# Optimization experiments

Measured on AMD Instinct MI355X. Metric: run time of the kernel, lower is better.

The kernel has to match this reference:

```python
import jax, jax.numpy as jnp
import numpy as np

N = 50000   # nodes
E = 640000  # edges
G = 256     # graphs
IN = 32     # in_channels
H = 128     # hidden_channels
L = 5       # num GENConv layers
LH = 64     # lstm hidden
OUT = 10    # out_channels
EPS_GEN = 1e-7

def _bn(x, g, b, eps=1e-5):
    # BatchNorm1d in training mode: biased batch stats over node dim
    mu = x.mean(0)
    var = x.var(0)
    return (x - mu) * jax.lax.rsqrt(var + eps) * g + b

def _genconv(x, eattr, src, dst, w1, b1, g1, bb1, w2, b2):
    # message: relu(x_j + edge_attr) + eps   [E, H]
    msg = jax.nn.relu(x[src] + eattr) + EPS_GEN
    # softmax aggregation (t=1) per destination node, per channel
    m = jax.ops.segment_max(msg, dst, num_segments=N)
    e = jnp.exp(msg - m[dst])
    s = jax.ops.segment_sum(e, dst, num_segments=N)
    alpha = e / s[dst]
    agg = jax.ops.segment_sum(alpha * msg, dst, num_segments=N)
    out = agg + x
    # MLP: Linear(H,2H) -> BN -> ReLU -> Linear(2H,H)
    hmid = jax.nn.relu(_bn(out @ w1.T + b1, g1, bb1))
    return hmid @ w2.T + b2

def setup_inputs() -> dict:
    key = jax.random.key(0)
    ks = jax.random.split(key, 16)
    s = 0.05
    inp = {}
    inp["x"] = jax.random.normal(ks[0], (N, IN), jnp.float32)
    inp["node_cycle_counts"] = jax.random.uniform(ks[1], (N, 8), jnp.float32)
    inp["edge_index"] = jax.random.randint(ks[2], (2, E), 0, N)
    inp["edge_attr"] = jax.random.randint(ks[3], (E,), 0, 4)
    inp["batch"] = jnp.sort(jax.random.randint(ks[4], (N,), 0, G))
    inp["fc_w"] = jax.random.normal(ks[5], (H, IN + 8), jnp.float32) * s
    inp["fc_b"] = jnp.zeros((H,), jnp.float32)
    inp["edge_emb"] = jax.random.normal(ks[6], (4, H), jnp.float32) * s
    inp["conv_w1"] = jax.random.normal(ks[7], (L, 2 * H, H), jnp.float32) * s
    inp["conv_b1"] = jnp.zeros((L, 2 * H), jnp.float32)
    inp["conv_bn_g"] = jnp.ones((L, 2 * H), jnp.float32)
    inp["conv_bn_b"] = jnp.zeros((L, 2 * H), jnp.float32)
    inp["conv_w2"] = jax.random.normal(ks[8], (L, H, 2 * H), jnp.float32) * s
    inp["conv_b2"] = jnp.zeros((L, H), jnp.float32)
    inp["bn_g"] = jnp.ones((L, H), jnp.float32)
    inp["bn_b"] = jnp.zeros((L, H), jnp.float32)
    inp["lstm_wih"] = jax.random.normal(ks[9], (4 * LH, H), jnp.float32) * s
    inp["lstm_whh"] = jax.random.normal(ks[10], (4 * LH, LH), jnp.float32) * s
    inp["lstm_bih"] = jnp.zeros((4 * LH,), jnp.float32)
    inp["lstm_bhh"] = jnp.zeros((4 * LH,), jnp.float32)
    inp["lin_w"] = jax.random.normal(ks[11], (OUT, LH), jnp.float32) * s
    inp["lin_b"] = jnp.zeros((OUT,), jnp.float32)
    return inp

def reference(x, node_cycle_counts, edge_index, edge_attr, batch,
              fc_w, fc_b, edge_emb, conv_w1, conv_b1, conv_bn_g, conv_bn_b,
              conv_w2, conv_b2, bn_g, bn_b,
              lstm_wih, lstm_whh, lstm_bih, lstm_bhh, lin_w, lin_b):
    src, dst = edge_index[0], edge_index[1]
    eattr = edge_emb[edge_attr]                              # [E, H]
    h = jnp.concatenate([x, node_cycle_counts], 1) @ fc_w.T + fc_b  # [N, H]
    for i in range(L):
        h = _genconv(h, eattr, src, dst, conv_w1[i], conv_b1[i],
                     conv_bn_g[i], conv_bn_b[i], conv_w2[i], conv_b2[i])
        h = jax.nn.relu(_bn(h, bn_g[i], bn_b[i]))
    p = jax.ops.segment_sum(h, batch, num_segments=G)        # global_add_pool [G, H]
    # single-step LSTM with h0 = c0 = 0
    gates = p @ lstm_wih.T + lstm_bih + lstm_bhh
    i_g, f_g, g_g, o_g = jnp.split(gates, 4, axis=1)
    c = jax.nn.sigmoid(i_g) * jnp.tanh(g_g)
    hh = jax.nn.sigmoid(o_g) * jnp.tanh(c)
    return hh @ lin_w.T + lin_b                              # [G, OUT]
```

## Files before the change

kernel.cpp:

```cpp
#include <hip/hip_runtime.h>
#include <hip/hip_bf16.h>
#include <math.h>

#define NNODES 50000
#define NEDGES 640000
#define NGRAPH 256
#define CIN 32
#define HD 128
#define NLAYER 5
#define LHID 64
#define COUT 10
#define EPS_GEN 1e-7f
#define INVN (1.f / (float)NNODES)
#define SCAN_BLOCKS 196

typedef __attribute__((ext_vector_type(8))) short short8;
typedef __attribute__((ext_vector_type(4))) float floatx4;

__device__ __forceinline__ unsigned short f2bf(float f) {
    union { float f; unsigned u; } v; v.f = f;
    unsigned r = v.u + 0x7FFFu + ((v.u >> 16) & 1u);
    return (unsigned short)(r >> 16);
}
__device__ __forceinline__ float bf2f(unsigned short h) {
    union { unsigned u; float f; } v; v.u = ((unsigned)h) << 16;
    return v.f;
}

__global__ void hist_kernel(const int* __restrict__ dst, int* __restrict__ deg, int e) {
    int i = blockIdx.x * blockDim.x + threadIdx.x;
    if (i < e) atomicAdd(&deg[dst[i]], 1);
}

__global__ void blocksum_kernel(const int* __restrict__ deg, int* __restrict__ bsum) {
    int i = blockIdx.x * 256 + threadIdx.x;
    int v = (i < NNODES) ? deg[i] : 0;
#pragma unroll
    for (int d = 32; d; d >>= 1) v += __shfl_down(v, d);
    __shared__ int ws4[4];
    if ((threadIdx.x & 63) == 0) ws4[threadIdx.x >> 6] = v;
    __syncthreads();
    if (threadIdx.x == 0) bsum[blockIdx.x] = ws4[0] + ws4[1] + ws4[2] + ws4[3];
}

__global__ void scanpartials_kernel(const int* __restrict__ bsum, int* __restrict__ bpre) {
    __shared__ int t[256];
    int i = threadIdx.x;
    t[i] = (i < SCAN_BLOCKS) ? bsum[i] : 0;
    __syncthreads();
    for (int d = 1; d < 256; d <<= 1) {
        int v = (i >= d) ? t[i - d] : 0;
        __syncthreads();
        t[i] += v;
        __syncthreads();
    }
    bpre[i] = (i == 0) ? 0 : t[i - 1];
}

__global__ void writeoff_kernel(const int* __restrict__ deg, const int* __restrict__ bpre,
                                int* __restrict__ off, int* __restrict__ cursor) {
    __shared__ int t[256];
    int tid = threadIdx.x;
    int i = blockIdx.x * 256 + tid;
    int v = (i < NNODES) ? deg[i] : 0;
    t[tid] = v;
    __syncthreads();
    for (int d = 1; d < 256; d <<= 1) {
        int u = (tid >= d) ? t[tid - d] : 0;
        __syncthreads();
        t[tid] += u;
        __syncthreads();
    }
    int excl = bpre[blockIdx.x] + t[tid] - v;
    if (i < NNODES) { off[i] = excl; cursor[i] = excl; }
    if (i == NNODES - 1) off[NNODES] = excl + v;
}

__global__ void scatter_kernel(const int* __restrict__ src, const int* __restrict__ dst,
                               const int* __restrict__ eattr, int* __restrict__ cursor,
                               int* __restrict__ pedge, int e) {
    int i = blockIdx.x * blockDim.x + threadIdx.x;
    if (i < e) {
        int slot = atomicAdd(&cursor[dst[i]], 1);
        pedge[slot] = src[i] | (eattr[i] << 27);
    }
}

__global__ void wsplit_kernel(const float* __restrict__ w1, const float* __restrict__ w2,
                              short* __restrict__ w1h, short* __restrict__ w1l,
                              short* __restrict__ w2h, short* __restrict__ w2l) {
    int i = blockIdx.x * 256 + threadIdx.x;
    if (i < NLAYER * 2 * HD * HD) {
        float v = w1[i];
        unsigned short hb = f2bf(v);
        w1h[i] = (short)hb;
        w1l[i] = (short)f2bf(v - bf2f(hb));
        float u = w2[i];
        unsigned short hb2 = f2bf(u);
        w2h[i] = (short)hb2;
        w2l[i] = (short)f2bf(u - bf2f(hb2));
    }
}

__global__ __launch_bounds__(256) void fc_kernel(
    const float* __restrict__ x, const float* __restrict__ ncc,
    const float* __restrict__ w, const float* __restrict__ b,
    float* __restrict__ h) {
    __shared__ float ws[HD][41];
    __shared__ float bs[HD];
    int tid = threadIdx.x;
    for (int i = tid; i < HD * 40; i += 256) ws[i / 40][i % 40] = w[i];
    if (tid < HD) bs[tid] = b[tid];
    __syncthreads();
    int c = tid & 127;
    int hi = tid >> 7;
#pragma unroll
    for (int nn = 0; nn < 4; ++nn) {
        int node = blockIdx.x * 8 + nn * 2 + hi;
        const float4* xr = reinterpret_cast<const float4*>(x + (size_t)node * CIN);
        const float4* nr = reinterpret_cast<const float4*>(ncc + (size_t)node * 8);
        float acc = bs[c];
#pragma unroll
        for (int k4 = 0; k4 < 8; ++k4) {
            float4 xv = xr[k4];
            acc += xv.x * ws[c][k4 * 4 + 0];
            acc += xv.y * ws[c][k4 * 4 + 1];
            acc += xv.z * ws[c][k4 * 4 + 2];
            acc += xv.w * ws[c][k4 * 4 + 3];
        }
#pragma unroll
        for (int k4 = 0; k4 < 2; ++k4) {
            float4 nv = nr[k4];
            acc += nv.x * ws[c][32 + k4 * 4 + 0];
            acc += nv.y * ws[c][32 + k4 * 4 + 1];
            acc += nv.z * ws[c][32 + k4 * 4 + 2];
            acc += nv.w * ws[c][32 + k4 * 4 + 3];
        }
        h[(size_t)node * HD + c] = acc;
    }
}

template <bool BN>
__global__ __launch_bounds__(256) void agg_kernel(
    const float* __restrict__ h, const int* __restrict__ off,
    const int* __restrict__ pedge, const float* __restrict__ edge_emb,
    const float* __restrict__ sums, const float* __restrict__ sqs,
    const float* __restrict__ g, const float* __restrict__ bb,
    short* __restrict__ x0h, short* __restrict__ x0l) {
    __shared__ float ee[4 * HD];
    __shared__ float scs[HD], shs[HD];
    int tid = threadIdx.x;
    ee[tid] = edge_emb[tid];
    ee[tid + 256] = edge_emb[tid + 256];
    if (BN && tid < HD) {
        float mu = sums[tid] * INVN;
        float var = fmaxf(sqs[tid] * INVN - mu * mu, 0.f);
        float is = rsqrtf(var + 1e-5f);
        float sc = g[tid] * is;
        scs[tid] = sc;
        shs[tid] = bb[tid] - mu * sc;
    }
    __syncthreads();

    int node = blockIdx.x * 4 + (tid >> 6);
    int lane = tid & 63;
    int half = lane >> 5;
    int c4 = (lane & 31) * 4;

    int b = off[node], e = off[node + 1];
    float4 sc4 = make_float4(1.f, 1.f, 1.f, 1.f);
    float4 sh4 = make_float4(0.f, 0.f, 0.f, 0.f);
    if (BN) {
        sc4 = *reinterpret_cast<const float4*>(&scs[c4]);
        sh4 = *reinterpret_cast<const float4*>(&shs[c4]);
    }
    float4 S = make_float4(0.f, 0.f, 0.f, 0.f);
    float4 T = make_float4(0.f, 0.f, 0.f, 0.f);
    int j = b + half;
    unsigned pnext = (j < e) ? (unsigned)pedge[j] : 0u;
    for (; j < e; j += 2) {
        unsigned p = pnext;
        if (j + 2 < e) pnext = (unsigned)pedge[j + 2];
        int s = p & 0x07FFFFFFu;
        int a = p >> 27;
        float4 v = *reinterpret_cast<const float4*>(&h[(size_t)s * HD + c4]);
        float4 ev = *reinterpret_cast<const float4*>(&ee[a * HD + c4]);
        if (BN) {
            v.x = fmaxf(fmaf(v.x, sc4.x, sh4.x), 0.f);
            v.y = fmaxf(fmaf(v.y, sc4.y, sh4.y), 0.f);
            v.z = fmaxf(fmaf(v.z, sc4.z, sh4.z), 0.f);
            v.w = fmaxf(fmaf(v.w, sc4.w, sh4.w), 0.f);
        }
        float m0 = fmaxf(v.x + ev.x, 0.f) + EPS_GEN;
        float m1 = fmaxf(v.y + ev.y, 0.f) + EPS_GEN;
        float m2 = fmaxf(v.z + ev.z, 0.f) + EPS_GEN;
        float m3 = fmaxf(v.w + ev.w, 0.f) + EPS_GEN;
        float e0 = __expf(m0), e1 = __expf(m1), e2 = __expf(m2), e3 = __expf(m3);
        S.x += e0; S.y += e1; S.z += e2; S.w += e3;
        T.x = fmaf(e0, m0, T.x); T.y = fmaf(e1, m1, T.y);
        T.z = fmaf(e2, m2, T.z); T.w = fmaf(e3, m3, T.w);
    }
    S.x += __shfl(S.x, lane ^ 32); S.y += __shfl(S.y, lane ^ 32);
    S.z += __shfl(S.z, lane ^ 32); S.w += __shfl(S.w, lane ^ 32);
    T.x += __shfl(T.x, lane ^ 32); T.y += __shfl(T.y, lane ^ 32);
    T.z += __shfl(T.z, lane ^ 32); T.w += __shfl(T.w, lane ^ 32);
    if (half == 0) {
        float4 r = *reinterpret_cast<const float4*>(&h[(size_t)node * HD + c4]);
        if (BN) {
            r.x = fmaxf(fmaf(r.x, sc4.x, sh4.x), 0.f);
            r.y = fmaxf(fmaf(r.y, sc4.y, sh4.y), 0.f);
            r.z = fmaxf(fmaf(r.z, sc4.z, sh4.z), 0.f);
            r.w = fmaxf(fmaf(r.w, sc4.w, sh4.w), 0.f);
        }
        if (e > b) {
            r.x += T.x / S.x; r.y += T.y / S.y;
            r.z += T.z / S.z; r.w += T.w / S.w;
        }
        float vv[4] = {r.x, r.y, r.z, r.w};
        short4 hv, lv;
        short hh4[4], ll4[4];
#pragma unroll
        for (int q = 0; q < 4; ++q) {
            unsigned short hb = f2bf(vv[q]);
            hh4[q] = (short)hb;
            ll4[q] = (short)f2bf(vv[q] - bf2f(hb));
        }
        hv.x = hh4[0]; hv.y = hh4[1]; hv.z = hh4[2]; hv.w = hh4[3];
        lv.x = ll4[0]; lv.y = ll4[1]; lv.z = ll4[2]; lv.w = ll4[3];
        *reinterpret_cast<short4*>(&x0h[(size_t)node * HD + c4]) = hv;
        *reinterpret_cast<short4*>(&x0l[(size_t)node * HD + c4]) = lv;
    }
}

template <int NPANEL, int KT, int NFULL, bool TRANS>
__global__ __launch_bounds__(256) void gemm_kernel(
    const short* __restrict__ Ahg, const short* __restrict__ Alg,
    const float* __restrict__ Afp,
    const short* __restrict__ Bhg, const short* __restrict__ Blg,
    const float* __restrict__ bias,
    const float* __restrict__ sums_in, const float* __restrict__ sqs_in,
    const float* __restrict__ g_in, const float* __restrict__ b_in,
    float* __restrict__ C, float* __restrict__ sums, float* __restrict__ sqs,
    int M) {
    constexpr int K = KT * 32;
    constexpr int BSTRIDE = K + 8;
    constexpr int NT = NPANEL / 16;
    __shared__ short Bs[2][NPANEL][BSTRIDE];
    __shared__ float scol[NPANEL], sqcol[NPANEL];
    __shared__ float sL[256], shL[256];
    int tid = threadIdx.x;
    int m0 = blockIdx.x * 128;
    int n0 = blockIdx.y * NPANEL;
    if (tid < NPANEL) { scol[tid] = 0.f; sqcol[tid] = 0.f; }
    if (TRANS && tid < K) {
        float mu = sums_in[tid] * INVN;
        float var = fmaxf(sqs_in[tid] * INVN - mu * mu, 0.f);
        float is = rsqrtf(var + 1e-5f);
        float sc = g_in[tid] * is;
        sL[tid] = sc;
        shL[tid] = b_in[tid] - mu * sc;
    }
    constexpr int ELEMS = NPANEL * (K / 8);
#pragma unroll
    for (int i = tid; i < ELEMS; i += 256) {
        int n = i / (K / 8);
        int k8 = (i % (K / 8)) * 8;
        *reinterpret_cast<short8*>(&Bs[0][n][k8]) =
            *reinterpret_cast<const short8*>(&Bhg[(size_t)(n0 + n) * K + k8]);
        *reinterpret_cast<short8*>(&Bs[1][n][k8]) =
            *reinterpret_cast<const short8*>(&Blg[(size_t)(n0 + n) * K + k8]);
    }
    __syncthreads();

    int wv = tid >> 6;
    int lane = tid & 63;
    int ml = lane & 15;
    int quad = lane >> 4;
    int mrow0 = m0 + wv * 32;

    floatx4 acc[2][NT];
#pragma unroll
    for (int mt = 0; mt < 2; ++mt)
#pragma unroll
        for (int nt = 0; nt < NT; ++nt) acc[mt][nt] = (floatx4){0.f, 0.f, 0.f, 0.f};

    int arow[2];
#pragma unroll
    for (int mt = 0; mt < 2; ++mt) arow[mt] = min(mrow0 + mt * 16 + ml, M - 1);

    if (!TRANS) {
        short8 ah[2][KT], al[2][KT];
#pragma unroll
        for (int mt = 0; mt < 2; ++mt)
#pragma unroll
            for (int kt = 0; kt < KT; ++kt) {
                size_t aoff = (size_t)arow[mt] * K + kt * 32 + quad * 8;
                ah[mt][kt] = *reinterpret_cast<const short8*>(&Ahg[aoff]);
                al[mt][kt] = *reinterpret_cast<const short8*>(&Alg[aoff]);
            }
#pragma unroll
        for (int kt = 0; kt < KT; ++kt)
#pragma unroll
            for (int nt = 0; nt < NT; ++nt) {
                short8 bh = *reinterpret_cast<const short8*>(&Bs[0][nt * 16 + ml][kt * 32 + quad * 8]);
                short8 bl = *reinterpret_cast<const short8*>(&Bs[1][nt * 16 + ml][kt * 32 + quad * 8]);
#pragma unroll
                for (int mt = 0; mt < 2; ++mt) {
                    acc[mt][nt] = __builtin_amdgcn_mfma_f32_16x16x32_bf16(ah[mt][kt], bh, acc[mt][nt], 0, 0, 0);
                    acc[mt][nt] = __builtin_amdgcn_mfma_f32_16x16x32_bf16(al[mt][kt], bh, acc[mt][nt], 0, 0, 0);
                    acc[mt][nt] = __builtin_amdgcn_mfma_f32_16x16x32_bf16(ah[mt][kt], bl, acc[mt][nt], 0, 0, 0);
                }
            }
    } else {
        short8 ah[2][2], al[2][2];
        auto loadA = [&](int kt, int buf) {
#pragma unroll
            for (int mt = 0; mt < 2; ++mt) {
                const float* ap = &Afp[(size_t)arow[mt] * K + kt * 32 + quad * 8];
                float4 v0 = *reinterpret_cast<const float4*>(ap);
                float4 v1 = *reinterpret_cast<const float4*>(ap + 4);
                int kg = kt * 32 + quad * 8;
                float4 s0 = *reinterpret_cast<const float4*>(&sL[kg]);
                float4 s1 = *reinterpret_cast<const float4*>(&sL[kg + 4]);
                float4 h0 = *reinterpret_cast<const float4*>(&shL[kg]);
                float4 h1 = *reinterpret_cast<const float4*>(&shL[kg + 4]);
                float vv[8] = {
                    fmaxf(fmaf(v0.x, s0.x, h0.x), 0.f), fmaxf(fmaf(v0.y, s0.y, h0.y), 0.f),
                    fmaxf(fmaf(v0.z, s0.z, h0.z), 0.f), fmaxf(fmaf(v0.w, s0.w, h0.w), 0.f),
                    fmaxf(fmaf(v1.x, s1.x, h1.x), 0.f), fmaxf(fmaf(v1.y, s1.y, h1.y), 0.f),
                    fmaxf(fmaf(v1.z, s1.z, h1.z), 0.f), fmaxf(fmaf(v1.w, s1.w, h1.w), 0.f)};
                short8 hv, lv;
#pragma unroll
                for (int q = 0; q < 8; ++q) {
                    unsigned short hb = f2bf(vv[q]);
                    hv[q] = (short)hb;
                    lv[q] = (short)f2bf(vv[q] - bf2f(hb));
                }
                ah[mt][buf] = hv;
                al[mt][buf] = lv;
            }
        };
        loadA(0, 0);
        for (int kt = 0; kt < KT; ++kt) {
            int cur = kt & 1;
            if (kt + 1 < KT) loadA(kt + 1, cur ^ 1);
#pragma unroll
            for (int nt = 0; nt < NT; ++nt) {
                short8 bh = *reinterpret_cast<const short8*>(&Bs[0][nt * 16 + ml][kt * 32 + quad * 8]);
                short8 bl = *reinterpret_cast<const short8*>(&Bs[1][nt * 16 + ml][kt * 32 + quad * 8]);
#pragma unroll
                for (int mt = 0; mt < 2; ++mt) {
                    acc[mt][nt] = __builtin_amdgcn_mfma_f32_16x16x32_bf16(ah[mt][cur], bh, acc[mt][nt], 0, 0, 0);
                    acc[mt][nt] = __builtin_amdgcn_mfma_f32_16x16x32_bf16(al[mt][cur], bh, acc[mt][nt], 0, 0, 0);
                    acc[mt][nt] = __builtin_amdgcn_mfma_f32_16x16x32_bf16(ah[mt][cur], bl, acc[mt][nt], 0, 0, 0);
                }
            }
        }
    }

#pragma unroll
    for (int nt = 0; nt < NT; ++nt) {
        int col = nt * 16 + ml;
        float bv = bias[n0 + col];
        float cs = 0.f, cq = 0.f;
#pragma unroll
        for (int mt = 0; mt < 2; ++mt)
#pragma unroll
            for (int r = 0; r < 4; ++r) {
                int m = mrow0 + mt * 16 + quad * 4 + r;
                if (m < M) {
                    float v = acc[mt][nt][r] + bv;
                    C[(size_t)m * NFULL + n0 + col] = v;
                    cs += v; cq += v * v;
                }
            }
        atomicAdd(&scol[col], cs);
        atomicAdd(&sqcol[col], cq);
    }
    __syncthreads();
    if (tid < NPANEL) {
        atomicAdd(&sums[n0 + tid], scol[tid]);
        atomicAdd(&sqs[n0 + tid], sqcol[tid]);
    }
}

__global__ void pool_kernel(const float* __restrict__ h, const int* __restrict__ batch,
                            const float* __restrict__ sums, const float* __restrict__ sqs,
                            const float* __restrict__ g, const float* __restrict__ bb,
                            float* __restrict__ p) {
    __shared__ int range[2];
    __shared__ float acc2[256];
    int gid = blockIdx.x;
    int tid = threadIdx.x;
    if (tid < 2) {
        int target = gid + tid;
        int lo = 0, hi = NNODES;
        while (lo < hi) {
            int mid = (lo + hi) >> 1;
            if (batch[mid] < target) lo = mid + 1; else hi = mid;
        }
        range[tid] = lo;
    }
    __syncthreads();
    int s0 = range[0], s1 = range[1];
    int c = tid & 127;
    int half = tid >> 7;
    float mu = sums[c] * INVN;
    float var = fmaxf(sqs[c] * INVN - mu * mu, 0.f);
    float is = rsqrtf(var + 1e-5f);
    float sc = g[c] * is;
    float sh = bb[c] - mu * sc;
    float a = 0.f;
    for (int r = s0 + half; r < s1; r += 2)
        a += fmaxf(fmaf(h[(size_t)r * HD + c], sc, sh), 0.f);
    acc2[tid] = a;
    __syncthreads();
    if (half == 0) p[gid * HD + c] = acc2[c] + acc2[c + 128];
}

__global__ void lstm_kernel(const float* __restrict__ p, const float* __restrict__ wih,
                            const float* __restrict__ bih, const float* __restrict__ bhh,
                            const float* __restrict__ lin_w, const float* __restrict__ lin_b,
                            float* __restrict__ out) {
    __shared__ float pr[HD];
    __shared__ float gates[4 * LHID];
    __shared__ float hh[LHID];
    int g = blockIdx.x;
    int t = threadIdx.x;
    if (t < HD) pr[t] = p[g * HD + t];
    __syncthreads();
    {
        float acc = bih[t] + bhh[t];
        const float* wr = wih + t * HD;
        for (int k = 0; k < HD; ++k) acc += pr[k] * wr[k];
        gates[t] = acc;
    }
    __syncthreads();
    if (t < LHID) {
        float ig = gates[t];
        float gg = gates[2 * LHID + t];
        float og = gates[3 * LHID + t];
        float c = (1.f / (1.f + __expf(-ig))) * tanhf(gg);
        hh[t] = (1.f / (1.f + __expf(-og))) * tanhf(c);
    }
    __syncthreads();
    if (t < COUT) {
        float acc = lin_b[t];
        const float* lr = lin_w + t * LHID;
        for (int k = 0; k < LHID; ++k) acc += hh[k] * lr[k];
        out[g * COUT + t] = acc;
    }
}

extern "C" void kernel_launch(void* const* d_in, const int* in_sizes, int n_in,
                              void* d_out, int out_size, void* d_ws, size_t ws_size,
                              hipStream_t stream) {
    const float* x        = (const float*)d_in[0];
    const float* ncc      = (const float*)d_in[1];
    const int*   eidx     = (const int*)d_in[2];
    const int*   eattr    = (const int*)d_in[3];
    const int*   batch    = (const int*)d_in[4];
    const float* fc_w     = (const float*)d_in[5];
    const float* fc_b     = (const float*)d_in[6];
    const float* edge_emb = (const float*)d_in[7];
    const float* conv_w1  = (const float*)d_in[8];
    const float* conv_b1  = (const float*)d_in[9];
    const float* conv_bn_g= (const float*)d_in[10];
    const float* conv_bn_b= (const float*)d_in[11];
    const float* conv_w2  = (const float*)d_in[12];
    const float* conv_b2  = (const float*)d_in[13];
    const float* bn_g     = (const float*)d_in[14];
    const float* bn_b     = (const float*)d_in[15];
    const float* lstm_wih = (const float*)d_in[16];
    const float* lstm_bih = (const float*)d_in[18];
    const float* lstm_bhh = (const float*)d_in[19];
    const float* lin_w    = (const float*)d_in[20];
    const float* lin_b    = (const float*)d_in[21];
    float* out = (float*)d_out;

    const int* src = eidx;
    const int* dst = eidx + NEDGES;

    char* ws = (char*)d_ws;
    size_t o = 0;
    auto alloc = [&](size_t bytes) {
        size_t r = o;
        o += (bytes + 255) & ~(size_t)255;
        return r;
    };
    int*   deg    = (int*)(ws + alloc(NNODES * 4));
    int*   off    = (int*)(ws + alloc((NNODES + 1) * 4));
    int*   cursor = (int*)(ws + alloc(NNODES * 4));
    int*   pedge  = (int*)(ws + alloc(NEDGES * 4));
    int*   bsum   = (int*)(ws + alloc(256 * 4));
    int*   bpre   = (int*)(ws + alloc(256 * 4));
    float* h      = (float*)(ws + alloc((size_t)NNODES * HD * 4));
    short* x0h    = (short*)(ws + alloc((size_t)NNODES * HD * 2));
    short* x0l    = (short*)(ws + alloc((size_t)NNODES * HD * 2));
    float* xmid   = (float*)(ws + alloc((size_t)NNODES * 2 * HD * 4));
    short* w1h    = (short*)(ws + alloc((size_t)NLAYER * 2 * HD * HD * 2));
    short* w1l    = (short*)(ws + alloc((size_t)NLAYER * 2 * HD * HD * 2));
    short* w2h    = (short*)(ws + alloc((size_t)NLAYER * 2 * HD * HD * 2));
    short* w2l    = (short*)(ws + alloc((size_t)NLAYER * 2 * HD * HD * 2));
    float* stats  = (float*)(ws + alloc(NLAYER * 768 * 4));
    float* p      = (float*)(ws + alloc((size_t)NGRAPH * HD * 4));

    hipMemsetAsync(deg, 0, NNODES * 4, stream);
    hipMemsetAsync(stats, 0, NLAYER * 768 * 4, stream);
    hist_kernel<<<(NEDGES + 255) / 256, 256, 0, stream>>>(dst, deg, NEDGES);
    blocksum_kernel<<<SCAN_BLOCKS, 256, 0, stream>>>(deg, bsum);
    scanpartials_kernel<<<1, 256, 0, stream>>>(bsum, bpre);
    writeoff_kernel<<<SCAN_BLOCKS, 256, 0, stream>>>(deg, bpre, off, cursor);
    scatter_kernel<<<(NEDGES + 255) / 256, 256, 0, stream>>>(src, dst, eattr, cursor, pedge, NEDGES);
    wsplit_kernel<<<(NLAYER * 2 * HD * HD + 255) / 256, 256, 0, stream>>>(
        conv_w1, conv_w2, w1h, w1l, w2h, w2l);

    fc_kernel<<<NNODES / 8, 256, 0, stream>>>(x, ncc, fc_w, fc_b, h);

    const int gemmGridX = (NNODES + 127) / 128;
    for (int l = 0; l < NLAYER; ++l) {
        float* sumsA = stats + l * 768;
        float* sqsA  = sumsA + 256;
        float* sumsB = sumsA + 512;
        float* sqsB  = sumsA + 640;
        if (l == 0)
            agg_kernel<false><<<NNODES / 4, 256, 0, stream>>>(
                h, off, pedge, edge_emb, nullptr, nullptr, nullptr, nullptr, x0h, x0l);
        else {
            float* pB = stats + (l - 1) * 768;
            agg_kernel<true><<<NNODES / 4, 256, 0, stream>>>(
                h, off, pedge, edge_emb, pB + 512, pB + 640,
                bn_g + (l - 1) * HD, bn_b + (l - 1) * HD, x0h, x0l);
        }
        gemm_kernel<128, 4, 256, false><<<dim3(gemmGridX, 2), 256, 0, stream>>>(
            x0h, x0l, nullptr,
            w1h + (size_t)l * 2 * HD * HD, w1l + (size_t)l * 2 * HD * HD,
            conv_b1 + l * 2 * HD,
            nullptr, nullptr, nullptr, nullptr,
            xmid, sumsA, sqsA, NNODES);
        gemm_kernel<64, 8, 128, true><<<dim3(gemmGridX, 2), 256, 0, stream>>>(
            nullptr, nullptr, xmid,
            w2h + (size_t)l * 2 * HD * HD, w2l + (size_t)l * 2 * HD * HD,
            conv_b2 + l * HD,
            sumsA, sqsA, conv_bn_g + l * 2 * HD, conv_bn_b + l * 2 * HD,
            h, sumsB, sqsB, NNODES);
    }

    {
        float* pB = stats + (NLAYER - 1) * 768;
        pool_kernel<<<NGRAPH, 256, 0, stream>>>(h, batch, pB + 512, pB + 640,
                                                bn_g + (NLAYER - 1) * HD,
                                                bn_b + (NLAYER - 1) * HD, p);
    }

    lstm_kernel<<<NGRAPH, 256, 0, stream>>>(p, lstm_wih, lstm_bih, lstm_bhh, lin_w, lin_b, out);
}
```

Before: 971.9 us.

## Sort nodes by degree for aggregation, unroll edge loop, swap GEMM grid order

Adds a counting sort of nodes by in-degree, computed once, and the aggregation kernel reads nodes through this permutation so each block handles nodes of similar degree. This is meant to reduce wavefront imbalance. The edge loop is unrolled to issue two gather loads per iteration, and the self-row load is moved ahead of the loop to overlap latency. The GEMM grid is transposed so both N-panels of the same M tile run next to each other, which should improve L2 reuse of the A rows. The permutation scatters nodes across blocks, which may hurt locality of the x0 writes, and it adds three small setup kernels.

```diff
diff --git a/kernel.cpp b/kernel.cpp
--- a/kernel.cpp
+++ b/kernel.cpp
@@ -83,6 +83,34 @@
     if (i < e) {
         int slot = atomicAdd(&cursor[dst[i]], 1);
         pedge[slot] = src[i] | (eattr[i] << 27);
+    }
+}
+
+__global__ void dhist_kernel(const int* __restrict__ deg, int* __restrict__ dh) {
+    int i = blockIdx.x * 256 + threadIdx.x;
+    if (i < NNODES) atomicAdd(&dh[min(deg[i], 255)], 1);
+}
+
+__global__ void dscan_kernel(const int* __restrict__ dh, int* __restrict__ dcur) {
+    __shared__ int t[256];
+    int i = threadIdx.x;
+    t[i] = dh[i];
+    __syncthreads();
+    for (int d = 1; d < 256; d <<= 1) {
+        int v = (i >= d) ? t[i - d] : 0;
+        __syncthreads();
+        t[i] += v;
+        __syncthreads();
+    }
+    dcur[i] = (i == 0) ? 0 : t[i - 1];
+}
+
+__global__ void dscatter_kernel(const int* __restrict__ deg, int* __restrict__ dcur,
+                                int* __restrict__ perm) {
+    int i = blockIdx.x * 256 + threadIdx.x;
+    if (i < NNODES) {
+        int slot = atomicAdd(&dcur[min(deg[i], 255)], 1);
+        perm[slot] = i;
     }
 }
 
@@ -144,6 +172,7 @@
 __global__ __launch_bounds__(256) void agg_kernel(
     const float* __restrict__ h, const int* __restrict__ off,
     const int* __restrict__ pedge, const float* __restrict__ edge_emb,
+    const int* __restrict__ perm,
     const float* __restrict__ sums, const float* __restrict__ sqs,
     const float* __restrict__ g, const float* __restrict__ bb,
     short* __restrict__ x0h, short* __restrict__ x0l) {
@@ -162,7 +191,7 @@
     }
     __syncthreads();
 
-    int node = blockIdx.x * 4 + (tid >> 6);
+    int node = perm[blockIdx.x * 4 + (tid >> 6)];
     int lane = tid & 63;
     int half = lane >> 5;
     int c4 = (lane & 31) * 4;
@@ -174,38 +203,59 @@
         sc4 = *reinterpret_cast<const float4*>(&scs[c4]);
         sh4 = *reinterpret_cast<const float4*>(&shs[c4]);
     }
+    float4 r = *reinterpret_cast<const float4*>(&h[(size_t)node * HD + c4]);
+
     float4 S = make_float4(0.f, 0.f, 0.f, 0.f);
     float4 T = make_float4(0.f, 0.f, 0.f, 0.f);
-    int j = b + half;
-    unsigned pnext = (j < e) ? (unsigned)pedge[j] : 0u;
-    for (; j < e; j += 2) {
-        unsigned p = pnext;
-        if (j + 2 < e) pnext = (unsigned)pedge[j + 2];
-        int s = p & 0x07FFFFFFu;
-        int a = p >> 27;
-        float4 v = *reinterpret_cast<const float4*>(&h[(size_t)s * HD + c4]);
-        float4 ev = *reinterpret_cast<const float4*>(&ee[a * HD + c4]);
+    for (int j = b + half; j < e; j += 4) {
+        int j2 = j + 2;
+        bool has2 = j2 < e;
+        unsigned p0 = (unsigned)pedge[j];
+        unsigned p1 = (unsigned)pedge[has2 ? j2 : j];
+        int s0 = p0 & 0x07FFFFFFu, a0 = p0 >> 27;
+        int s1 = p1 & 0x07FFFFFFu, a1 = p1 >> 27;
+        float4 v0 = *reinterpret_cast<const float4*>(&h[(size_t)s0 * HD + c4]);
+        float4 v1 = *reinterpret_cast<const float4*>(&h[(size_t)s1 * HD + c4]);
+        float4 e0 = *reinterpret_cast<const float4*>(&ee[a0 * HD + c4]);
+        float4 e1 = *reinterpret_cast<const float4*>(&ee[a1 * HD + c4]);
         if (BN) {
-            v.x = fmaxf(fmaf(v.x, sc4.x, sh4.x), 0.f);
-            v.y = fmaxf(fmaf(v.y, sc4.y, sh4.y), 0.f);
-            v.z = fmaxf(fmaf(v.z, sc4.z, sh4.z), 0.f);
-            v.w = fmaxf(fmaf(v.w, sc4.w, sh4.w), 0.f);
-        }
-        float m0 = fmaxf(v.x + ev.x, 0.f) + EPS_GEN;
-        float m1 = fmaxf(v.y + ev.y, 0.f) + EPS_GEN;
-        float m2 = fmaxf(v.z + ev.z, 0.f) + EPS_GEN;
-        float m3 = fmaxf(v.w + ev.w, 0.f) + EPS_GEN;
-        float e0 = __expf(m0), e1 = __expf(m1), e2 = __expf(m2), e3 = __expf(m3);
-        S.x += e0; S.y += e1; S.z += e2; S.w += e3;
-        T.x = fmaf(e0, m0, T.x); T.y = fmaf(e1, m1, T.y);
-        T.z = fmaf(e2, m2, T.z); T.w = fmaf(e3, m3, T.w);
+            v0.x = fmaxf(fmaf(v0.x, sc4.x, sh4.x), 0.f);
+            v0.y = fmaxf(fmaf(v0.y, sc4.y, sh4.y), 0.f);
+            v0.z = fmaxf(fmaf(v0.z, sc4.z, sh4.z), 0.f);
+            v0.w = fmaxf(fmaf(v0.w, sc4.w, sh4.w), 0.f);
+        }
+        {
+            float m0 = fmaxf(v0.x + e0.x, 0.f) + EPS_GEN;
+            float m1 = fmaxf(v0.y + e0.y, 0.f) + EPS_GEN;
+            float m2 = fmaxf(v0.z + e0.z, 0.f) + EPS_GEN;
+            float m3 = fmaxf(v0.w + e0.w, 0.f) + EPS_GEN;
+            float x0_ = __expf(m0), x1_ = __expf(m1), x2_ = __expf(m2), x3_ = __expf(m3);
+            S.x += x0_; S.y += x1_; S.z += x2_; S.w += x3_;
+            T.x = fmaf(x0_, m0, T.x); T.y = fmaf(x1_, m1, T.y);
+            T.z = fmaf(x2_, m2, T.z); T.w = fmaf(x3_, m3, T.w);
+        }
+        if (has2) {
+            if (BN) {
+                v1.x = fmaxf(fmaf(v1.x, sc4.x, sh4.x), 0.f);
+                v1.y = fmaxf(fmaf(v1.y, sc4.y, sh4.y), 0.f);
+                v1.z = fmaxf(fmaf(v1.z, sc4.z, sh4.z), 0.f);
+                v1.w = fmaxf(fmaf(v1.w, sc4.w, sh4.w), 0.f);
+            }
+            float m0 = fmaxf(v1.x + e1.x, 0.f) + EPS_GEN;
+            float m1 = fmaxf(v1.y + e1.y, 0.f) + EPS_GEN;
+            float m2 = fmaxf(v1.z + e1.z, 0.f) + EPS_GEN;
+            float m3 = fmaxf(v1.w + e1.w, 0.f) + EPS_GEN;
+            float x0_ = __expf(m0), x1_ = __expf(m1), x2_ = __expf(m2), x3_ = __expf(m3);
+            S.x += x0_; S.y += x1_; S.z += x2_; S.w += x3_;
+            T.x = fmaf(x0_, m0, T.x); T.y = fmaf(x1_, m1, T.y);
+            T.z = fmaf(x2_, m2, T.z); T.w = fmaf(x3_, m3, T.w);
+        }
     }
     S.x += __shfl(S.x, lane ^ 32); S.y += __shfl(S.y, lane ^ 32);
     S.z += __shfl(S.z, lane ^ 32); S.w += __shfl(S.w, lane ^ 32);
     T.x += __shfl(T.x, lane ^ 32); T.y += __shfl(T.y, lane ^ 32);
     T.z += __shfl(T.z, lane ^ 32); T.w += __shfl(T.w, lane ^ 32);
     if (half == 0) {
-        float4 r = *reinterpret_cast<const float4*>(&h[(size_t)node * HD + c4]);
         if (BN) {
             r.x = fmaxf(fmaf(r.x, sc4.x, sh4.x), 0.f);
             r.y = fmaxf(fmaf(r.y, sc4.y, sh4.y), 0.f);
@@ -249,8 +299,8 @@
     __shared__ float scol[NPANEL], sqcol[NPANEL];
     __shared__ float sL[256], shL[256];
     int tid = threadIdx.x;
-    int m0 = blockIdx.x * 128;
-    int n0 = blockIdx.y * NPANEL;
+    int m0 = blockIdx.y * 128;
+    int n0 = blockIdx.x * NPANEL;
     if (tid < NPANEL) { scol[tid] = 0.f; sqcol[tid] = 0.f; }
     if (TRANS && tid < K) {
         float mu = sums_in[tid] * INVN;
@@ -494,6 +544,9 @@
     int*   pedge  = (int*)(ws + alloc(NEDGES * 4));
     int*   bsum   = (int*)(ws + alloc(256 * 4));
     int*   bpre   = (int*)(ws + alloc(256 * 4));
+    int*   dh     = (int*)(ws + alloc(256 * 4));
+    int*   dcur   = (int*)(ws + alloc(256 * 4));
+    int*   perm   = (int*)(ws + alloc(NNODES * 4));
     float* h      = (float*)(ws + alloc((size_t)NNODES * HD * 4));
     short* x0h    = (short*)(ws + alloc((size_t)NNODES * HD * 2));
     short* x0l    = (short*)(ws + alloc((size_t)NNODES * HD * 2));
@@ -506,18 +559,22 @@
     float* p      = (float*)(ws + alloc((size_t)NGRAPH * HD * 4));
 
     hipMemsetAsync(deg, 0, NNODES * 4, stream);
+    hipMemsetAsync(dh, 0, 256 * 4, stream);
     hipMemsetAsync(stats, 0, NLAYER * 768 * 4, stream);
     hist_kernel<<<(NEDGES + 255) / 256, 256, 0, stream>>>(dst, deg, NEDGES);
     blocksum_kernel<<<SCAN_BLOCKS, 256, 0, stream>>>(deg, bsum);
     scanpartials_kernel<<<1, 256, 0, stream>>>(bsum, bpre);
     writeoff_kernel<<<SCAN_BLOCKS, 256, 0, stream>>>(deg, bpre, off, cursor);
     scatter_kernel<<<(NEDGES + 255) / 256, 256, 0, stream>>>(src, dst, eattr, cursor, pedge, NEDGES);
+    dhist_kernel<<<SCAN_BLOCKS, 256, 0, stream>>>(deg, dh);
+    dscan_kernel<<<1, 256, 0, stream>>>(dh, dcur);
+    dscatter_kernel<<<SCAN_BLOCKS, 256, 0, stream>>>(deg, dcur, perm);
     wsplit_kernel<<<(NLAYER * 2 * HD * HD + 255) / 256, 256, 0, stream>>>(
         conv_w1, conv_w2, w1h, w1l, w2h, w2l);
 
     fc_kernel<<<NNODES / 8, 256, 0, stream>>>(x, ncc, fc_w, fc_b, h);
 
-    const int gemmGridX = (NNODES + 127) / 128;
+    const int gemmGridY = (NNODES + 127) / 128;
     for (int l = 0; l < NLAYER; ++l) {
         float* sumsA = stats + l * 768;
         float* sqsA  = sumsA + 256;
@@ -525,20 +582,20 @@
         float* sqsB  = sumsA + 640;
         if (l == 0)
             agg_kernel<false><<<NNODES / 4, 256, 0, stream>>>(
-                h, off, pedge, edge_emb, nullptr, nullptr, nullptr, nullptr, x0h, x0l);
+                h, off, pedge, edge_emb, perm, nullptr, nullptr, nullptr, nullptr, x0h, x0l);
         else {
             float* pB = stats + (l - 1) * 768;
             agg_kernel<true><<<NNODES / 4, 256, 0, stream>>>(
-                h, off, pedge, edge_emb, pB + 512, pB + 640,
+                h, off, pedge, edge_emb, perm, pB + 512, pB + 640,
                 bn_g + (l - 1) * HD, bn_b + (l - 1) * HD, x0h, x0l);
         }
-        gemm_kernel<128, 4, 256, false><<<dim3(gemmGridX, 2), 256, 0, stream>>>(
+        gemm_kernel<128, 4, 256, false><<<dim3(2, gemmGridY), 256, 0, stream>>>(
             x0h, x0l, nullptr,
             w1h + (size_t)l * 2 * HD * HD, w1l + (size_t)l * 2 * HD * HD,
             conv_b1 + l * 2 * HD,
             nullptr, nullptr, nullptr, nullptr,
             xmid, sumsA, sqsA, NNODES);
-        gemm_kernel<64, 8, 128, true><<<dim3(gemmGridX, 2), 256, 0, stream>>>(
+        gemm_kernel<64, 8, 128, true><<<dim3(2, gemmGridY), 256, 0, stream>>>(
             nullptr, nullptr, xmid,
             w2h + (size_t)l * 2 * HD * HD, w2l + (size_t)l * 2 * HD * HD,
             conv_b2 + l * HD,
```

Result: slower. 1.291 ms (+32.8%).
